# Optimization experiments

Hardware: AMD Instinct MI355X
Metric: run time of the kernel (lower is better)

The kernel has to match this reference:

```python
import jax, jax.numpy as jnp
import numpy as np

B = 1      # batch
D = 64     # octree grid side at this level
N = 65536  # active voxels
C = 32     # channels (nin == nout for resblock)
K = 3      # kernel size


def _offsets():
    r = jnp.arange(K) - K // 2
    oz, oy, ox = jnp.meshgrid(r, r, r, indexing='ij')
    return jnp.stack([oz.ravel(), oy.ravel(), ox.ravel()], axis=-1)  # [27,3] (kz,ky,kx order)


def octree_conv3d(values, indices, mask_values, kernel, bias, activation=None):
    # values: [N,Cin], indices: [N,4] (b,z,y,x), mask_values: [N,1]
    Cin = values.shape[-1]
    Cout = kernel.shape[-1]
    taps = kernel.reshape(K * K * K, Cin, Cout)            # kz,ky,kx order == kernel[kz,ky,kx]
    vals = jnp.einsum('nc,tcd->tnd', values, taps)         # [27,N,Cout]
    offs = _offsets()                                      # [27,3]
    coords = indices[:, 1:]                                # [N,3]
    # shift = [0, kz-1, ky-1, kx-1]; clamp to [0, D-1] (stride=inv_stride=1)
    sh = jnp.clip(coords[None, :, :] + offs[:, None, :], 0, D - 1)  # [27,N,3]
    lin = indices[:, 0][None, :] * (D * D * D) + sh[..., 0] * (D * D) + sh[..., 1] * D + sh[..., 2]
    grid = jnp.zeros((B * D * D * D, Cout), dtype=values.dtype)
    grid = grid.at[lin.reshape(-1)].add(vals.reshape(-1, Cout))     # scatter-add == coalesce sum
    out_lin = indices[:, 0] * (D * D * D) + coords[:, 0] * (D * D) + coords[:, 1] * D + coords[:, 2]
    gathered = grid[out_lin]                               # [N,Cout] values at mask positions
    out = (gathered + mask_values * bias[None, :]) * mask_values     # result + mask*bias; result*mask
    if activation is not None:
        out = activation(out)
    return out


def setup_inputs() -> dict:
    key = jax.random.key(0)
    k1, k2, k3, k4, k5, k6 = jax.random.split(key, 6)
    G = B * D * D * D
    perm = jax.random.permutation(k1, G)[:N]               # unique (coalesced) voxel indices
    b = perm // (D * D * D)
    rem = perm % (D * D * D)
    z = rem // (D * D)
    y = (rem // D) % D
    x = rem % D
    indices = jnp.stack([b, z, y, x], axis=-1).astype(jnp.int64)   # [N,4]
    values = jax.random.normal(k2, (N, C), dtype=jnp.float32)
    mask_values = jnp.ones((N, 1), dtype=jnp.float32)
    stdv = 1.0 / np.sqrt(K * K * K * C)
    kern1 = (jax.random.uniform(k3, (K, K, K, C, C)) - 0.5) * 2.0 * stdv
    bias1 = (jax.random.uniform(k4, (C,)) - 0.5) * 2.0 * stdv
    kern2 = (jax.random.uniform(k5, (K, K, K, C, C)) - 0.5) * 2.0 * stdv
    bias2 = (jax.random.uniform(k6, (C,)) - 0.5) * 2.0 * stdv
    return {'values': values, 'indices': indices, 'mask_values': mask_values,
            'kern1': kern1, 'bias1': bias1, 'kern2': kern2, 'bias2': bias2}


def reference(values, indices, mask_values, kern1, bias1, kern2, bias2):
    # OctreeResblock: conv(relu) -> conv -> residual add, all on the sparse index set
    h = octree_conv3d(values, indices, mask_values, kern1, bias1, activation=jax.nn.relu)
    h = octree_conv3d(h, indices, mask_values, kern2, bias2, activation=None)
    return values + h
```

## Files before the change

### kernel.cpp

```cpp
#include <hip/hip_runtime.h>

#define NPTS 65536
#define CCH  32
#define DDIM 64
#define GVOX (DDIM*DDIM*DDIM)
#define MAXT 2080

typedef _Float16 half8   __attribute__((ext_vector_type(8)));
typedef _Float16 half4v  __attribute__((ext_vector_type(4)));
typedef float    floatx16 __attribute__((ext_vector_type(16)));

__global__ __launch_bounds__(256) void k_prep0(
    int* __restrict__ map, int* __restrict__ sorted,
    const float* __restrict__ values, _Float16* __restrict__ valsh,
    const float* __restrict__ k1, const float* __restrict__ k2,
    _Float16* __restrict__ w1, _Float16* __restrict__ w2,
    _Float16* __restrict__ hh, int* __restrict__ pcoord,
    int* __restrict__ cnt, int* __restrict__ slot)
{
  int tid = blockIdx.x * 256 + threadIdx.x;
  if (tid < GVOX/4) { ((int4*)map)[tid] = make_int4(-1,-1,-1,-1); return; }
  tid -= GVOX/4;
  if (tid < MAXT*32/4) { ((int4*)sorted)[tid] = make_int4(NPTS,NPTS,NPTS,NPTS); return; }
  tid -= MAXT*32/4;
  if (tid < (NPTS*CCH)/4) {
    float4 v = ((const float4*)values)[tid];
    half4v h = { (_Float16)v.x, (_Float16)v.y, (_Float16)v.z, (_Float16)v.w };
    ((half4v*)valsh)[tid] = h; return;
  }
  tid -= (NPTS*CCH)/4;
  if (tid < 27*CCH*CCH) {
    int t = tid/(CCH*CCH), r = tid%(CCH*CCH);
    int cin = r/CCH, cout = r%CCH;
    int h = cin >> 4, kq = (cin >> 3) & 1, j = cin & 7;
    int dst = t*1024 + h*512 + (kq*32 + cout)*8 + j;
    w1[dst] = (_Float16)k1[tid]; w2[dst] = (_Float16)k2[tid]; return;
  }
  tid -= 27*CCH*CCH;
  if (tid < CCH) { valsh[NPTS*CCH+tid] = (_Float16)0.f; hh[NPTS*CCH+tid] = (_Float16)0.f; return; }
  tid -= CCH;
  if (tid < 27) { cnt[tid] = 0; slot[tid] = 0; return; }
  tid -= 27;
  if (tid == 0) pcoord[NPTS] = 0;
}
#define PREP0_THREADS (GVOX/4 + MAXT*32/4 + (NPTS*CCH)/4 + 27*CCH*CCH + CCH + 27 + 1)

__global__ __launch_bounds__(256) void k_prep1(const int* __restrict__ idx,
                                               int* __restrict__ map,
                                               int* __restrict__ pcoord,
                                               int* __restrict__ cls,
                                               int* __restrict__ cnt)
{
  __shared__ int lcnt[27];
  if (threadIdx.x < 27) lcnt[threadIdx.x] = 0;
  __syncthreads();
  const int n = blockIdx.x*256 + threadIdx.x;
  const int b = idx[4*n], z = idx[4*n+1], y = idx[4*n+2], x = idx[4*n+3];
  map[((b*DDIM + z)*DDIM + y)*DDIM + x] = n;
  pcoord[n] = (b<<18) | (z<<12) | (y<<6) | x;
  const int cz = (z==0)?0:((z==DDIM-1)?2:1);
  const int cy = (y==0)?0:((y==DDIM-1)?2:1);
  const int cx = (x==0)?0:((x==DDIM-1)?2:1);
  const int c = cz*9 + cy*3 + cx;
  cls[n] = c;
  atomicAdd(&lcnt[c], 1);
  __syncthreads();
  if (threadIdx.x < 27 && lcnt[threadIdx.x]) atomicAdd(&cnt[threadIdx.x], lcnt[threadIdx.x]);
}

__global__ void k_prep2(const int* __restrict__ cnt, int* __restrict__ clsbase,
                        int* __restrict__ tstart, int* __restrict__ ntiles)
{
  if (threadIdx.x == 0 && blockIdx.x == 0) {
    int b = 0, tb = 0;
    for (int c = 0; c < 27; ++c) {
      clsbase[c] = b; tstart[c] = tb;
      int nt = (cnt[c] + 31) >> 5;
      b += nt << 5; tb += nt;
    }
    tstart[27] = tb; *ntiles = tb;
  }
}

__global__ __launch_bounds__(256) void k_prep3(const int* __restrict__ cls,
                                               const int* __restrict__ clsbase,
                                               int* __restrict__ slot,
                                               int* __restrict__ sorted,
                                               const int* __restrict__ tstart,
                                               const int* __restrict__ ntp,
                                               int* __restrict__ tileclass)
{
  if (blockIdx.x < NPTS/256) {
    __shared__ int lcnt[27], lbase[27];
    if (threadIdx.x < 27) lcnt[threadIdx.x] = 0;
    __syncthreads();
    const int n = blockIdx.x*256 + threadIdx.x;
    const int c = cls[n];
    const int lrank = atomicAdd(&lcnt[c], 1);
    __syncthreads();
    if (threadIdx.x < 27)
      lbase[threadIdx.x] = lcnt[threadIdx.x] ? atomicAdd(&slot[threadIdx.x], lcnt[threadIdx.x]) : 0;
    __syncthreads();
    sorted[clsbase[c] + lbase[c] + lrank] = n;
  } else {
    const int i = (blockIdx.x - NPTS/256)*256 + threadIdx.x;
    if (i >= MAXT) return;
    const int nt = *ntp;
    int c = 13;
    if (i < nt) {
      for (int cc = 0; cc < 27; ++cc)
        if (i >= tstart[cc] && i < tstart[cc+1]) { c = cc; break; }
    }
    tileclass[i] = c;
  }
}

__global__ __launch_bounds__(256) void k_nbr(const int* __restrict__ sorted,
                                             const int* __restrict__ pcoord,
                                             const int* __restrict__ map,
                                             int* __restrict__ nbr)
{
  const int i = blockIdx.x*256 + threadIdx.x;
  if (i >= MAXT*32) return;
  const int tile = i >> 5, m = i & 31;
  const int pid = sorted[i];
  const int pc  = pcoord[pid];
  const int bb = pc>>18, z = (pc>>12)&63, y = (pc>>6)&63, x = pc&63;
  const int linb = bb << 18;
  const int az[3] = { max(z-1,0)<<12, z<<12, min(z+1,DDIM-1)<<12 };
  const int ay[3] = { max(y-1,0)<<6,  y<<6,  min(y+1,DDIM-1)<<6 };
  const int ax[3] = { max(x-1,0),     x,     min(x+1,DDIM-1) };
#pragma unroll
  for (int j = 0; j < 27; ++j) {
    int src = map[linb | az[j/9] | ay[(j/3)%3] | ax[j%3]];
    nbr[(tile*27 + j)*32 + m] = (src < 0) ? NPTS : src;
  }
}

template<int MODE>
__global__ __launch_bounds__(256) void conv32(
    const _Float16* __restrict__ A,
    const int* __restrict__ sorted,
    const int* __restrict__ tileclass,
    const int* __restrict__ nbr,
    const int* __restrict__ ntp,
    const _Float16* __restrict__ wfrag,
    const float* __restrict__ bias,
    const float* __restrict__ mask,
    const float* __restrict__ resid,
    _Float16* __restrict__ hout,
    float* __restrict__ fout)
{
  __shared__ _Float16 bs[27*1024];
  {
    const int4* s = (const int4*)wfrag;
    int4* d = (int4*)bs;
#pragma unroll
    for (int i = 0; i < 14; ++i) {
      const int o = threadIdx.x + i*256;
      if (o < 27*1024/8) d[o] = s[o];
    }
  }
  __syncthreads();

  const int tile = blockIdx.x*4 + (threadIdx.x >> 6);
  if (tile >= *ntp) return;
  const int lane = threadIdx.x & 63;
  const int m = lane & 31, kh = lane >> 5;
  const int scls = __builtin_amdgcn_readfirstlane(tileclass[tile]);
  const int cz = scls/9, cy = (scls/3)%3, cx = scls%3;

  int nb[27];
#pragma unroll
  for (int j = 0; j < 27; ++j) nb[j] = nbr[(tile*27 + j)*32 + m];

  floatx16 acc = {};
#pragma unroll
  for (int j = 0; j < 27; ++j) {
    const int jz = j/9, jy = (j/3)%3, jx = j%3;
    const int tz = (cz==1) ? (2-jz) : ((jz==1) ? 1 : ((cz==0) ? 0 : 2));
    const int ty = (cy==1) ? (2-jy) : ((jy==1) ? 1 : ((cy==0) ? 0 : 2));
    const int tx = (cx==1) ? (2-jx) : ((jx==1) ? 1 : ((cx==0) ? 0 : 2));
    const int t  = tz*9 + ty*3 + tx;
    const _Float16* ap = A + nb[j]*CCH + kh*8;
    half8 alo = *(const half8*)ap;
    half8 ahi = *(const half8*)(ap + 16);
    const _Float16* bp = bs + t*1024 + lane*8;
    half8 blo = *(const half8*)bp;
    half8 bhi = *(const half8*)(bp + 512);
    acc = __builtin_amdgcn_mfma_f32_32x32x16_f16(alo, blo, acc, 0, 0, 0);
    acc = __builtin_amdgcn_mfma_f32_32x32x16_f16(ahi, bhi, acc, 0, 0, 0);
  }

  const float bi = bias[m];
#pragma unroll
  for (int r = 0; r < 16; ++r) {
    const int row = (r&3) + 8*(r>>2) + 4*kh;
    const int pr  = sorted[tile*32 + row];
    if (pr >= NPTS) continue;
    const float mk = mask[pr];
    const float v = (acc[r] + mk*bi) * mk;
    if (MODE == 0) hout[pr*CCH + m] = (_Float16)fmaxf(v, 0.f);
    else           fout[pr*CCH + m] = resid[pr*CCH + m] + v;
  }
}


extern "C" void kernel_launch(void* const* d_in, const int* in_sizes, int n_in,
                              void* d_out, int out_size, void* d_ws, size_t ws_size,
                              hipStream_t stream) {
  const float* values = (const float*)d_in[0];
  const int*   indices= (const int*)  d_in[1];
  const float* maskv  = (const float*)d_in[2];
  const float* kern1  = (const float*)d_in[3];
  const float* bias1  = (const float*)d_in[4];
  const float* kern2  = (const float*)d_in[5];
  const float* bias2  = (const float*)d_in[6];
  float* out = (float*)d_out;

  char* ws = (char*)d_ws;
  size_t off = 0;
  auto alloc = [&](size_t bytes) { void* p = ws + off; off = (off + bytes + 255) & ~(size_t)255; return p; };
  int*      map      = (int*)     alloc(GVOX*4);
  int*      pcoord   = (int*)     alloc((NPTS+1)*4);
  int*      cls      = (int*)     alloc(NPTS*4);
  int*      sorted   = (int*)     alloc(MAXT*32*4);
  int*      tileclass= (int*)     alloc(MAXT*4);
  int*      nbr      = (int*)     alloc((size_t)MAXT*27*32*4);
  int*      cnt      = (int*)     alloc(27*4);
  int*      slot     = (int*)     alloc(27*4);
  int*      clsbase  = (int*)     alloc(27*4);
  int*      tstart   = (int*)     alloc(28*4);
  int*      ntiles   = (int*)     alloc(4);
  _Float16* valsh    = (_Float16*)alloc((NPTS+1)*CCH*2);
  _Float16* hh       = (_Float16*)alloc((NPTS+1)*CCH*2);
  _Float16* wf1      = (_Float16*)alloc(27*1024*2);
  _Float16* wf2      = (_Float16*)alloc(27*1024*2);

  k_prep0<<<(PREP0_THREADS + 255)/256, 256, 0, stream>>>(
      map, sorted, values, valsh, kern1, kern2, wf1, wf2, hh, pcoord, cnt, slot);
  k_prep1<<<NPTS/256, 256, 0, stream>>>(indices, map, pcoord, cls, cnt);
  k_prep2<<<1, 64, 0, stream>>>(cnt, clsbase, tstart, ntiles);
  k_prep3<<<NPTS/256 + (MAXT+255)/256, 256, 0, stream>>>(
      cls, clsbase, slot, sorted, tstart, ntiles, tileclass);
  k_nbr  <<<(MAXT*32)/256, 256, 0, stream>>>(sorted, pcoord, map, nbr);

  conv32<0><<<MAXT/4, 256, 0, stream>>>(valsh, sorted, tileclass, nbr, ntiles,
                                        wf1, bias1, maskv, nullptr, hh, nullptr);
  conv32<1><<<MAXT/4, 256, 0, stream>>>(hh, sorted, tileclass, nbr, ntiles,
                                        wf2, bias2, maskv, values, nullptr, out);
}
```

Baseline: 151.9 us.

## Fuse preprocessing kernels and compute neighbor lookups inside conv kernels

Merges the prep kernels into a setup kernel and a sort kernel, with per-block prefix computation of class bases in shared memory. Map initialization moves to hipMemsetAsync, and counters are stored as -1-based slots after the map. The materialized neighbor table and the k_nbr pass are removed; each conv kernel recomputes neighbor indices from the hash map directly. This cuts launches and the global traffic for the neighbor array, but the map gathers are now done twice, once in each conv. The early exit on tile count is also dropped and relies on padded tiles.

```diff
diff --git a/kernel.cpp b/kernel.cpp
--- a/kernel.cpp
+++ b/kernel.cpp
@@ -10,18 +10,39 @@
 typedef _Float16 half4v  __attribute__((ext_vector_type(4)));
 typedef float    floatx16 __attribute__((ext_vector_type(16)));
 
-__global__ __launch_bounds__(256) void k_prep0(
-    int* __restrict__ map, int* __restrict__ sorted,
+
+__global__ __launch_bounds__(256) void k_setup(
+    const int* __restrict__ idx, int* __restrict__ map, int* __restrict__ cnt,
+    int* __restrict__ pcoord, int* __restrict__ cls, int* __restrict__ sorted,
     const float* __restrict__ values, _Float16* __restrict__ valsh,
     const float* __restrict__ k1, const float* __restrict__ k2,
     _Float16* __restrict__ w1, _Float16* __restrict__ w2,
-    _Float16* __restrict__ hh, int* __restrict__ pcoord,
-    int* __restrict__ cnt, int* __restrict__ slot)
+    _Float16* __restrict__ hh)
 {
-  int tid = blockIdx.x * 256 + threadIdx.x;
-  if (tid < GVOX/4) { ((int4*)map)[tid] = make_int4(-1,-1,-1,-1); return; }
-  tid -= GVOX/4;
-  if (tid < MAXT*32/4) { ((int4*)sorted)[tid] = make_int4(NPTS,NPTS,NPTS,NPTS); return; }
+  if (blockIdx.x < NPTS/256) {
+    __shared__ int lcnt[27];
+    if (threadIdx.x < 27) lcnt[threadIdx.x] = 0;
+    __syncthreads();
+    const int n = blockIdx.x*256 + threadIdx.x;
+    const int4 q = ((const int4*)idx)[n];
+    const int b = q.x, z = q.y, y = q.z, x = q.w;
+    const int pk = (b<<18)|(z<<12)|(y<<6)|x;
+    map[pk] = n;
+    pcoord[n] = pk;
+    const int cz = (z==0)?0:((z==DDIM-1)?2:1);
+    const int cy = (y==0)?0:((y==DDIM-1)?2:1);
+    const int cx = (x==0)?0:((x==DDIM-1)?2:1);
+    const int c = cz*9 + cy*3 + cx;
+    cls[n] = c;
+    atomicAdd(&lcnt[c], 1);
+    __syncthreads();
+    if (threadIdx.x < 27 && lcnt[threadIdx.x]) atomicAdd(&cnt[threadIdx.x], lcnt[threadIdx.x]);
+    return;
+  }
+  int tid = (blockIdx.x - NPTS/256)*256 + threadIdx.x;
+  if (tid < MAXT*32/4) {
+    ((int4*)sorted)[tid] = make_int4(NPTS,NPTS,NPTS,NPTS); return;
+  }
   tid -= MAXT*32/4;
   if (tid < (NPTS*CCH)/4) {
     float4 v = ((const float4*)values)[tid];
@@ -39,111 +60,57 @@
   tid -= 27*CCH*CCH;
   if (tid < CCH) { valsh[NPTS*CCH+tid] = (_Float16)0.f; hh[NPTS*CCH+tid] = (_Float16)0.f; return; }
   tid -= CCH;
-  if (tid < 27) { cnt[tid] = 0; slot[tid] = 0; return; }
-  tid -= 27;
   if (tid == 0) pcoord[NPTS] = 0;
 }
-#define PREP0_THREADS (GVOX/4 + MAXT*32/4 + (NPTS*CCH)/4 + 27*CCH*CCH + CCH + 27 + 1)
-
-__global__ __launch_bounds__(256) void k_prep1(const int* __restrict__ idx,
-                                               int* __restrict__ map,
-                                               int* __restrict__ pcoord,
-                                               int* __restrict__ cls,
-                                               int* __restrict__ cnt)
+#define SETUP_TAIL (MAXT*32/4 + (NPTS*CCH)/4 + 27*CCH*CCH + CCH + 1)
+#define SETUP_BLOCKS (NPTS/256 + (SETUP_TAIL + 255)/256)
+
+__global__ __launch_bounds__(256) void k_sort(
+    const int* __restrict__ cls, int* __restrict__ cs ,
+    int* __restrict__ sorted, int* __restrict__ tileclass)
 {
-  __shared__ int lcnt[27];
-  if (threadIdx.x < 27) lcnt[threadIdx.x] = 0;
+  __shared__ int scnt[27], clsbase[27], tstart[28], lcnt[27], lbase[27];
+  if (threadIdx.x < 27) { lcnt[threadIdx.x] = 0; scnt[threadIdx.x] = cs[threadIdx.x] + 1; }
   __syncthreads();
-  const int n = blockIdx.x*256 + threadIdx.x;
-  const int b = idx[4*n], z = idx[4*n+1], y = idx[4*n+2], x = idx[4*n+3];
-  map[((b*DDIM + z)*DDIM + y)*DDIM + x] = n;
-  pcoord[n] = (b<<18) | (z<<12) | (y<<6) | x;
-  const int cz = (z==0)?0:((z==DDIM-1)?2:1);
-  const int cy = (y==0)?0:((y==DDIM-1)?2:1);
-  const int cx = (x==0)?0:((x==DDIM-1)?2:1);
-  const int c = cz*9 + cy*3 + cx;
-  cls[n] = c;
-  atomicAdd(&lcnt[c], 1);
-  __syncthreads();
-  if (threadIdx.x < 27 && lcnt[threadIdx.x]) atomicAdd(&cnt[threadIdx.x], lcnt[threadIdx.x]);
-}
-
-__global__ void k_prep2(const int* __restrict__ cnt, int* __restrict__ clsbase,
-                        int* __restrict__ tstart, int* __restrict__ ntiles)
-{
-  if (threadIdx.x == 0 && blockIdx.x == 0) {
+  if (threadIdx.x == 0) {
     int b = 0, tb = 0;
     for (int c = 0; c < 27; ++c) {
       clsbase[c] = b; tstart[c] = tb;
-      int nt = (cnt[c] + 31) >> 5;
+      int nt = (scnt[c] + 31) >> 5;
       b += nt << 5; tb += nt;
     }
-    tstart[27] = tb; *ntiles = tb;
-  }
-}
-
-__global__ __launch_bounds__(256) void k_prep3(const int* __restrict__ cls,
-                                               const int* __restrict__ clsbase,
-                                               int* __restrict__ slot,
-                                               int* __restrict__ sorted,
-                                               const int* __restrict__ tstart,
-                                               const int* __restrict__ ntp,
-                                               int* __restrict__ tileclass)
-{
+    tstart[27] = tb;
+  }
+  __syncthreads();
   if (blockIdx.x < NPTS/256) {
-    __shared__ int lcnt[27], lbase[27];
-    if (threadIdx.x < 27) lcnt[threadIdx.x] = 0;
-    __syncthreads();
     const int n = blockIdx.x*256 + threadIdx.x;
     const int c = cls[n];
     const int lrank = atomicAdd(&lcnt[c], 1);
     __syncthreads();
     if (threadIdx.x < 27)
-      lbase[threadIdx.x] = lcnt[threadIdx.x] ? atomicAdd(&slot[threadIdx.x], lcnt[threadIdx.x]) : 0;
+      lbase[threadIdx.x] = lcnt[threadIdx.x] ? (atomicAdd(&cs[32+threadIdx.x], lcnt[threadIdx.x]) + 1) : 0;
     __syncthreads();
     sorted[clsbase[c] + lbase[c] + lrank] = n;
   } else {
     const int i = (blockIdx.x - NPTS/256)*256 + threadIdx.x;
     if (i >= MAXT) return;
-    const int nt = *ntp;
     int c = 13;
-    if (i < nt) {
+    if (i < tstart[27]) {
       for (int cc = 0; cc < 27; ++cc)
         if (i >= tstart[cc] && i < tstart[cc+1]) { c = cc; break; }
     }
     tileclass[i] = c;
   }
 }
-
-__global__ __launch_bounds__(256) void k_nbr(const int* __restrict__ sorted,
-                                             const int* __restrict__ pcoord,
-                                             const int* __restrict__ map,
-                                             int* __restrict__ nbr)
-{
-  const int i = blockIdx.x*256 + threadIdx.x;
-  if (i >= MAXT*32) return;
-  const int tile = i >> 5, m = i & 31;
-  const int pid = sorted[i];
-  const int pc  = pcoord[pid];
-  const int bb = pc>>18, z = (pc>>12)&63, y = (pc>>6)&63, x = pc&63;
-  const int linb = bb << 18;
-  const int az[3] = { max(z-1,0)<<12, z<<12, min(z+1,DDIM-1)<<12 };
-  const int ay[3] = { max(y-1,0)<<6,  y<<6,  min(y+1,DDIM-1)<<6 };
-  const int ax[3] = { max(x-1,0),     x,     min(x+1,DDIM-1) };
-#pragma unroll
-  for (int j = 0; j < 27; ++j) {
-    int src = map[linb | az[j/9] | ay[(j/3)%3] | ax[j%3]];
-    nbr[(tile*27 + j)*32 + m] = (src < 0) ? NPTS : src;
-  }
-}
+#define SORT_BLOCKS (NPTS/256 + (MAXT + 255)/256)
 
 template<int MODE>
 __global__ __launch_bounds__(256) void conv32(
     const _Float16* __restrict__ A,
+    const int* __restrict__ map,
+    const int* __restrict__ pcoord,
     const int* __restrict__ sorted,
     const int* __restrict__ tileclass,
-    const int* __restrict__ nbr,
-    const int* __restrict__ ntp,
     const _Float16* __restrict__ wfrag,
     const float* __restrict__ bias,
     const float* __restrict__ mask,
@@ -164,15 +131,25 @@
   __syncthreads();
 
   const int tile = blockIdx.x*4 + (threadIdx.x >> 6);
-  if (tile >= *ntp) return;
   const int lane = threadIdx.x & 63;
   const int m = lane & 31, kh = lane >> 5;
   const int scls = __builtin_amdgcn_readfirstlane(tileclass[tile]);
   const int cz = scls/9, cy = (scls/3)%3, cx = scls%3;
 
-  int nb[27];
-#pragma unroll
-  for (int j = 0; j < 27; ++j) nb[j] = nbr[(tile*27 + j)*32 + m];
+  const int pid = sorted[tile*32 + m];
+  const int pc  = pcoord[pid];
+  const int z = (pc>>12)&63, y = (pc>>6)&63, x = pc&63;
+  const int linb = pc & ~0x3FFFF;
+  const int az[3] = { max(z-1,0)<<12, z<<12, min(z+1,DDIM-1)<<12 };
+  const int ay[3] = { max(y-1,0)<<6,  y<<6,  min(y+1,DDIM-1)<<6 };
+  const int ax[3] = { max(x-1,0),     x,     min(x+1,DDIM-1) };
+
+  int srcs[27];
+#pragma unroll
+  for (int j = 0; j < 27; ++j) {
+    int s = map[linb | az[j/9] | ay[(j/3)%3] | ax[j%3]];
+    srcs[j] = (s < 0) ? NPTS : s;
+  }
 
   floatx16 acc = {};
 #pragma unroll
@@ -182,7 +159,7 @@
     const int ty = (cy==1) ? (2-jy) : ((jy==1) ? 1 : ((cy==0) ? 0 : 2));
     const int tx = (cx==1) ? (2-jx) : ((jx==1) ? 1 : ((cx==0) ? 0 : 2));
     const int t  = tz*9 + ty*3 + tx;
-    const _Float16* ap = A + nb[j]*CCH + kh*8;
+    const _Float16* ap = A + srcs[j]*CCH + kh*8;
     half8 alo = *(const half8*)ap;
     half8 ahi = *(const half8*)(ap + 16);
     const _Float16* bp = bs + t*1024 + lane*8;
@@ -221,32 +198,26 @@
   char* ws = (char*)d_ws;
   size_t off = 0;
   auto alloc = [&](size_t bytes) { void* p = ws + off; off = (off + bytes + 255) & ~(size_t)255; return p; };
-  int*      map      = (int*)     alloc(GVOX*4);
+  int*      map      = (int*)     alloc(GVOX*4 + 64*4);
+  int*      cntslot  = map + GVOX;
   int*      pcoord   = (int*)     alloc((NPTS+1)*4);
   int*      cls      = (int*)     alloc(NPTS*4);
   int*      sorted   = (int*)     alloc(MAXT*32*4);
   int*      tileclass= (int*)     alloc(MAXT*4);
-  int*      nbr      = (int*)     alloc((size_t)MAXT*27*32*4);
-  int*      cnt      = (int*)     alloc(27*4);
-  int*      slot     = (int*)     alloc(27*4);
-  int*      clsbase  = (int*)     alloc(27*4);
-  int*      tstart   = (int*)     alloc(28*4);
-  int*      ntiles   = (int*)     alloc(4);
   _Float16* valsh    = (_Float16*)alloc((NPTS+1)*CCH*2);
   _Float16* hh       = (_Float16*)alloc((NPTS+1)*CCH*2);
   _Float16* wf1      = (_Float16*)alloc(27*1024*2);
   _Float16* wf2      = (_Float16*)alloc(27*1024*2);
 
-  k_prep0<<<(PREP0_THREADS + 255)/256, 256, 0, stream>>>(
-      map, sorted, values, valsh, kern1, kern2, wf1, wf2, hh, pcoord, cnt, slot);
-  k_prep1<<<NPTS/256, 256, 0, stream>>>(indices, map, pcoord, cls, cnt);
-  k_prep2<<<1, 64, 0, stream>>>(cnt, clsbase, tstart, ntiles);
-  k_prep3<<<NPTS/256 + (MAXT+255)/256, 256, 0, stream>>>(
-      cls, clsbase, slot, sorted, tstart, ntiles, tileclass);
-  k_nbr  <<<(MAXT*32)/256, 256, 0, stream>>>(sorted, pcoord, map, nbr);
-
-  conv32<0><<<MAXT/4, 256, 0, stream>>>(valsh, sorted, tileclass, nbr, ntiles,
+  hipMemsetAsync(map, 0xFF, GVOX*4 + 64*4, stream);
+
+  k_setup<<<SETUP_BLOCKS, 256, 0, stream>>>(
+      indices, map, cntslot, pcoord, cls, sorted, values, valsh,
+      kern1, kern2, wf1, wf2, hh);
+  k_sort<<<SORT_BLOCKS, 256, 0, stream>>>(cls, cntslot, sorted, tileclass);
+
+  conv32<0><<<MAXT/4, 256, 0, stream>>>(valsh, map, pcoord, sorted, tileclass,
                                         wf1, bias1, maskv, nullptr, hh, nullptr);
-  conv32<1><<<MAXT/4, 256, 0, stream>>>(hh, sorted, tileclass, nbr, ntiles,
+  conv32<1><<<MAXT/4, 256, 0, stream>>>(hh, map, pcoord, sorted, tileclass,
                                         wf2, bias2, maskv, values, nullptr, out);
 }
```

Measured after the change: 153.1 us. Within noise of the previous version (+0.8%).
